# Kernel tuning notes

Hardware: AMD Instinct MI355X
Metric: run time of the kernel (lower is better)

The kernel has to match this reference:

```python
import jax, jax.numpy as jnp
import numpy as np
import itertools
jax.config.update("jax_enable_x64", True)

ND, NQ, B = 4, 3, 256          # ndrives, nqubits, batch_size
D = 2 ** NQ                     # Hilbert-space dim = 8


def _pauli_basis(nq):
    I = np.eye(2, dtype=np.complex128)
    X = np.array([[0, 1], [1, 0]], dtype=np.complex128)
    Y = np.array([[0, -1j], [1j, 0]], dtype=np.complex128)
    Z = np.array([[1, 0], [0, -1]], dtype=np.complex128)
    mats = []
    for combo in itertools.product([I, X, Y, Z], repeat=nq):
        m = np.array([[1.0 + 0j]], dtype=np.complex128)
        for s in combo:
            m = np.kron(m, s)
        mats.append(m)
    return np.stack(mats)  # [4**nq, 2**nq, 2**nq], Hermitian


def setup_inputs() -> dict:
    key = jax.random.key(0)
    k1, k2, k3 = jax.random.split(key, 3)
    paulies = jnp.asarray(_pauli_basis(NQ))          # [64, 8, 8] complex128
    L = paulies.shape[0]
    x = jax.random.normal(k1, (B, ND), dtype=jnp.float64)
    # keras 'normal' initializer ~ stddev 0.05
    kernel = 0.05 * jax.random.normal(k2, (ND, L), dtype=jnp.float64)
    bias = 0.05 * jax.random.normal(k3, (L,), dtype=jnp.float64)
    return {"x": x, "kernel": kernel, "bias": bias, "paulies": paulies}


def _probs(pw_i, paulies):
    # pw_i: [L] real pauli weights for one sample
    H = jnp.tensordot(pw_i.astype(jnp.complex128), paulies, axes=[[0], [0]])  # [D, D]
    e, v = jnp.linalg.eigh(H)                      # Hermitian eigendecomp
    expe = jnp.exp(-1j * e)                        # [D]
    # amp_j = sum_s conj(v)[0,s] * exp(-i e_s) * v[j,s]  (evolution of |0>)
    amp = jnp.einsum('s,js->j', jnp.conj(v[0, :]) * expe, v)  # [D]
    return amp.real ** 2 + amp.imag ** 2           # P, [D] float64


def reference(x, kernel, bias, paulies):
    pw = x @ kernel + bias                         # [B, L]
    f = lambda p: _probs(p, paulies)
    P = jax.vmap(f)(pw)                            # [B, D]
    # per-sample Jacobian dP/d(pauli_weights): [B, D, L]
    g = jax.vmap(jax.jacrev(f))(pw)
    oneoverp = 1.0 / P                             # [B, D]
    # chain rule: pw = x @ kernel + bias  =>  dP/dkernel[i,p,j,k] = x[i,j] * g[i,p,k]
    p_k = jnp.einsum('ij,ipk->ipjk', x, g)         # [B, D, ND, L]
    I_k = jnp.einsum('ipjk,iplm,ip->ijklm', p_k, p_k, oneoverp)  # [B, ND, L, ND, L]
    I_b = jnp.einsum('ipj,ipk,ip->ijk', g, g, oneoverp)          # [B, L, L]
    return (I_k, I_b)
```

## Files before the change

kernel.cpp:

```cpp
#include <hip/hip_runtime.h>
#include <math.h>

typedef float f4_t __attribute__((ext_vector_type(4)));

#define NTERM 26
#define TROW  9
#define TMAT  (TROW * 8)

__device__ __forceinline__ double rdin(const void* p, int idx, bool isdbl) {
  return isdbl ? ((const double*)p)[idx] : (double)((const float*)p)[idx];
}

__device__ __forceinline__ bool detect_dbl(const void* xv) {
  const float* xq = (const float*)xv;
  bool isdbl = false;
  for (int j = 0; j < 64; ++j) {
    float a = fabsf(xq[j]);
    if (!(a < 1e6f)) isdbl = true;
  }
  return isdbl;
}

__global__ __launch_bounds__(256) void fi_all(
    const void* __restrict__ xv,
    const void* __restrict__ kv,
    const void* __restrict__ bv,
    float* __restrict__ out, int Bn)
{
  const int wg   = blockIdx.x;
  const int i    = wg >> 2;
  const int jblk = wg & 3;
  const int t    = threadIdx.x;

  __shared__ float  pw[64];
  __shared__ float2 Zl[8][8];
  __shared__ float  invfact[56];
  __shared__ float2 Tall[NTERM * TMAT];
  __shared__ float2 Rl[NTERM][8];
  __shared__ float2 Ql[8][8][8];
  __shared__ float  ampre[8], ampim[8], invPs[8];
  __shared__ float  gk_t[8][64];
  __shared__ float  hk_t[8][68];

  const bool isdbl = detect_dbl(xv);

  if (t < 64) {
    float acc = (float)rdin(bv, t, isdbl);
    #pragma unroll
    for (int j = 0; j < 4; ++j)
      acc += (float)rdin(xv, i*4 + j, isdbl) * (float)rdin(kv, j*64 + t, isdbl);
    pw[t] = acc;
  } else if (t < 64 + 52) {
    int n = t - 64;
    float f = 1.0f;
    for (int u = 2; u <= n; ++u) f /= (float)u;
    invfact[n] = f;
  }
  __syncthreads();

  if (t < 64) {
    int r = t >> 3, c = t & 7;
    int m = r ^ c;
    float hre = 0.0f, him = 0.0f;
    for (int u = 0; u < 8; ++u) {
      int k = 0;
      float pr = 1.0f, pim = 0.0f;
      #pragma unroll
      for (int q = 0; q < 3; ++q) {
        int bit = 2 - q;
        int f  = (m >> bit) & 1;
        int ch = (u >> bit) & 1;
        int rb = (r >> bit) & 1;
        int d  = f ? (ch ? 2 : 1) : (ch ? 3 : 0);
        k = (k << 2) | d;
        if (d == 2) {
          float nr = rb ? -pim : pim;
          float ni = rb ?  pr  : -pr;
          pr = nr; pim = ni;
        } else if (d == 3 && rb) { pr = -pr; pim = -pim; }
      }
      float w = pw[k];
      hre += w * pr; him += w * pim;
    }
    Zl[r][c] = make_float2(him, -hre);
  }
  __syncthreads();

  if (t < 64) {
    const int r = t >> 3, c = t & 7;
    float2 Zrow[8];
    #pragma unroll
    for (int u = 0; u < 8; ++u) Zrow[u] = Zl[r][u];
    float Tre = (r == c) ? 1.0f : 0.0f;
    float Tim = 0.0f;
    Tall[r*TROW + c] = make_float2(Tre, Tim);
    #pragma unroll
    for (int j = 1; j < NTERM; ++j) {
      float cr[8], ci[8];
      #pragma unroll
      for (int u = 0; u < 8; ++u) {
        int srcl = (((u << 3) | c) << 2);
        cr[u] = __int_as_float(__builtin_amdgcn_ds_bpermute(srcl, __float_as_int(Tre)));
        ci[u] = __int_as_float(__builtin_amdgcn_ds_bpermute(srcl, __float_as_int(Tim)));
      }
      float nr = 0.0f, ni = 0.0f;
      #pragma unroll
      for (int u = 0; u < 8; ++u) {
        nr += Zrow[u].x*cr[u] - Zrow[u].y*ci[u];
        ni += Zrow[u].x*ci[u] + Zrow[u].y*cr[u];
      }
      Tre = nr; Tim = ni;
      Tall[j*TMAT + r*TROW + c] = make_float2(nr, ni);
    }
  }
  __syncthreads();

  if (t < NTERM * 8) {
    const int l = t >> 3, b = t & 7;
    float sr = 0.0f, si = 0.0f;
    for (int j = 0; j < NTERM; ++j) {
      float cf = invfact[j + l + 1];
      float2 a = Tall[j*TMAT + b*TROW];
      sr += cf * a.x; si += cf * a.y;
    }
    Rl[l][b] = make_float2(sr, si);
  }
  if (t < 8) {
    float ar = 0.0f, ai = 0.0f;
    for (int j = 0; j < NTERM; ++j) {
      float cf = invfact[j];
      float2 a = Tall[j*TMAT + t*TROW];
      ar += cf * a.x; ai += cf * a.y;
    }
    ampre[t] = ar; ampim[t] = ai;
    float P = ar*ar + ai*ai;
    invPs[t] = 1.0f / fmaxf(P, 1e-30f);
  }
  __syncthreads();

  {
    const int p  = t >> 5;
    const int a  = (t >> 2) & 7;
    const int b0 = (t & 3) << 1;
    float q0r = 0.f, q0i = 0.f, q1r = 0.f, q1i = 0.f;
    for (int l = 0; l < NTERM; ++l) {
      float2 T  = Tall[l*TMAT + p*TROW + a];
      float2 r0 = Rl[l][b0];
      float2 r1 = Rl[l][b0+1];
      q0r += T.x*r0.x - T.y*r0.y;  q0i += T.x*r0.y + T.y*r0.x;
      q1r += T.x*r1.x - T.y*r1.y;  q1i += T.x*r1.y + T.y*r1.x;
    }
    Ql[p][a][b0]   = make_float2(q0r, q0i);
    Ql[p][a][b0+1] = make_float2(q1r, q1i);
  }
  __syncthreads();

  if (t < 64) {
    const int k = t;
    const int d0 = (k >> 4) & 3, d1 = (k >> 2) & 3, d2 = k & 3;
    const int m = ((((d0 == 1) | (d0 == 2)) ? 1 : 0) << 2)
                | ((((d1 == 1) | (d1 == 2)) ? 1 : 0) << 1)
                |  (((d2 == 1) | (d2 == 2)) ? 1 : 0);
    float Sr[8], Si[8];
    #pragma unroll
    for (int p = 0; p < 8; ++p) { Sr[p] = 0.0f; Si[p] = 0.0f; }
    #pragma unroll
    for (int a = 0; a < 8; ++a) {
      float pr = 1.0f, pim = 0.0f;
      const int dd[3] = {d0, d1, d2};
      #pragma unroll
      for (int q = 0; q < 3; ++q) {
        int rb = (a >> (2 - q)) & 1;
        int d = dd[q];
        if (d == 2) {
          float nr = rb ? -pim : pim;
          float ni = rb ?  pr  : -pr;
          pr = nr; pim = ni;
        } else if (d == 3 && rb) { pr = -pr; pim = -pim; }
      }
      const int b = a ^ m;
      #pragma unroll
      for (int p = 0; p < 8; ++p) {
        float2 q2 = Ql[p][a][b];
        Sr[p] += pr*q2.x - pim*q2.y;
        Si[p] += pr*q2.y + pim*q2.x;
      }
    }
    #pragma unroll
    for (int p = 0; p < 8; ++p) {
      float gg = 2.0f * (ampre[p]*Si[p] - ampim[p]*Sr[p]);
      gk_t[p][k] = gg;
      hk_t[p][k] = gg * invPs[p];
    }
  }

  float xsc[4];
  {
    float xj = (float)rdin(xv, i*4 + jblk, isdbl);
    #pragma unroll
    for (int l = 0; l < 4; ++l)
      xsc[l] = xj * (float)rdin(xv, i*4 + l, isdbl);
  }
  __syncthreads();

  {
    const int m4  = (t & 15) << 2;
    const int g16 = t >> 4;
    float* okj = out + (size_t)i * 65536 + (size_t)jblk * 16384;
    float* ob  = out + (size_t)Bn * 65536 + (size_t)i * 4096;
    #pragma unroll
    for (int it = 0; it < 4; ++it) {
      const int k = it*16 + g16;
      f4_t acc = {0.f, 0.f, 0.f, 0.f};
      #pragma unroll
      for (int p = 0; p < 8; ++p) {
        float gv = gk_t[p][k];
        const f4_t hv = *(const f4_t*)&hk_t[p][m4];
        acc.x += gv*hv.x; acc.y += gv*hv.y; acc.z += gv*hv.z; acc.w += gv*hv.w;
      }
      if (jblk == 0)
        __builtin_nontemporal_store(acc, (f4_t*)(ob + (size_t)k*64 + m4));
      #pragma unroll
      for (int l = 0; l < 4; ++l) {
        f4_t vv = {xsc[l]*acc.x, xsc[l]*acc.y, xsc[l]*acc.z, xsc[l]*acc.w};
        __builtin_nontemporal_store(vv,
            (f4_t*)(okj + (size_t)k*256 + (size_t)l*64 + m4));
      }
    }
  }
}

extern "C" void kernel_launch(void* const* d_in, const int* in_sizes, int n_in,
                              void* d_out, int out_size, void* d_ws, size_t ws_size,
                              hipStream_t stream) {
  (void)n_in; (void)d_ws; (void)ws_size; (void)out_size;
  int Bn = in_sizes[0] / 4;
  fi_all<<<Bn * 4, 256, 0, stream>>>(d_in[0], d_in[1], d_in[2], (float*)d_out, Bn);
}
```

Baseline: 100.7 us.

## Cut Taylor terms, rotate solver wave per block, spread gradient stage over all waves

Reduces the Taylor series for the matrix exponential from 26 to 22 terms, which shrinks the serial T-power chain and the table sizes. Rotates which wavefront runs the serial setup so the four blocks per sample do not all load the same SIMD. Splits the gradient-contraction stage across all four waves, two Pauli rows each, instead of one wave doing all eight. The factorial loop now uses the hardware reciprocal. Fewer terms and the approximate reciprocal could cost accuracy if the Hamiltonian norm is large.

```diff
diff --git a/kernel.cpp b/kernel.cpp
--- a/kernel.cpp
+++ b/kernel.cpp
@@ -3,7 +3,7 @@
 
 typedef float f4_t __attribute__((ext_vector_type(4)));
 
-#define NTERM 26
+#define NTERM 22
 #define TROW  9
 #define TMAT  (TROW * 8)
 
@@ -31,10 +31,13 @@
   const int i    = wg >> 2;
   const int jblk = wg & 3;
   const int t    = threadIdx.x;
+  const int wv   = t >> 6;
+  const int tl   = t & 63;
+  const bool solver = (wv == jblk);
 
   __shared__ float  pw[64];
   __shared__ float2 Zl[8][8];
-  __shared__ float  invfact[56];
+  __shared__ float  invfact[48];
   __shared__ float2 Tall[NTERM * TMAT];
   __shared__ float2 Rl[NTERM][8];
   __shared__ float2 Ql[8][8][8];
@@ -44,22 +47,22 @@
 
   const bool isdbl = detect_dbl(xv);
 
-  if (t < 64) {
-    float acc = (float)rdin(bv, t, isdbl);
+  if (solver) {
+    float acc = (float)rdin(bv, tl, isdbl);
     #pragma unroll
     for (int j = 0; j < 4; ++j)
-      acc += (float)rdin(xv, i*4 + j, isdbl) * (float)rdin(kv, j*64 + t, isdbl);
-    pw[t] = acc;
-  } else if (t < 64 + 52) {
-    int n = t - 64;
+      acc += (float)rdin(xv, i*4 + j, isdbl) * (float)rdin(kv, j*64 + tl, isdbl);
+    pw[tl] = acc;
+  } else if (wv == ((jblk + 1) & 3) && tl < 48) {
+    int n = tl;
     float f = 1.0f;
-    for (int u = 2; u <= n; ++u) f /= (float)u;
+    for (int u = 2; u <= n; ++u) f *= __builtin_amdgcn_rcpf((float)u);
     invfact[n] = f;
   }
   __syncthreads();
 
-  if (t < 64) {
-    int r = t >> 3, c = t & 7;
+  if (solver) {
+    int r = tl >> 3, c = tl & 7;
     int m = r ^ c;
     float hre = 0.0f, him = 0.0f;
     for (int u = 0; u < 8; ++u) {
@@ -86,8 +89,8 @@
   }
   __syncthreads();
 
-  if (t < 64) {
-    const int r = t >> 3, c = t & 7;
+  if (solver) {
+    const int r = tl >> 3, c = tl & 7;
     float2 Zrow[8];
     #pragma unroll
     for (int u = 0; u < 8; ++u) Zrow[u] = Zl[r][u];
@@ -125,16 +128,17 @@
     }
     Rl[l][b] = make_float2(sr, si);
   }
-  if (t < 8) {
+  if (t >= 192 && t < 200) {
+    const int b = t - 192;
     float ar = 0.0f, ai = 0.0f;
     for (int j = 0; j < NTERM; ++j) {
       float cf = invfact[j];
-      float2 a = Tall[j*TMAT + t*TROW];
+      float2 a = Tall[j*TMAT + b*TROW];
       ar += cf * a.x; ai += cf * a.y;
     }
-    ampre[t] = ar; ampim[t] = ai;
+    ampre[b] = ar; ampim[b] = ai;
     float P = ar*ar + ai*ai;
-    invPs[t] = 1.0f / fmaxf(P, 1e-30f);
+    invPs[b] = 1.0f / fmaxf(P, 1e-30f);
   }
   __syncthreads();
 
@@ -155,15 +159,15 @@
   }
   __syncthreads();
 
-  if (t < 64) {
-    const int k = t;
+  {
+    const int k  = t & 63;
+    const int pg = t >> 6;
+    const int p0 = pg << 1, p1 = p0 + 1;
     const int d0 = (k >> 4) & 3, d1 = (k >> 2) & 3, d2 = k & 3;
     const int m = ((((d0 == 1) | (d0 == 2)) ? 1 : 0) << 2)
                 | ((((d1 == 1) | (d1 == 2)) ? 1 : 0) << 1)
                 |  (((d2 == 1) | (d2 == 2)) ? 1 : 0);
-    float Sr[8], Si[8];
-    #pragma unroll
-    for (int p = 0; p < 8; ++p) { Sr[p] = 0.0f; Si[p] = 0.0f; }
+    float S0r = 0.f, S0i = 0.f, S1r = 0.f, S1i = 0.f;
     #pragma unroll
     for (int a = 0; a < 8; ++a) {
       float pr = 1.0f, pim = 0.0f;
@@ -179,19 +183,15 @@
         } else if (d == 3 && rb) { pr = -pr; pim = -pim; }
       }
       const int b = a ^ m;
-      #pragma unroll
-      for (int p = 0; p < 8; ++p) {
-        float2 q2 = Ql[p][a][b];
-        Sr[p] += pr*q2.x - pim*q2.y;
-        Si[p] += pr*q2.y + pim*q2.x;
-      }
-    }
-    #pragma unroll
-    for (int p = 0; p < 8; ++p) {
-      float gg = 2.0f * (ampre[p]*Si[p] - ampim[p]*Sr[p]);
-      gk_t[p][k] = gg;
-      hk_t[p][k] = gg * invPs[p];
-    }
+      float2 qa = Ql[p0][a][b];
+      float2 qb = Ql[p1][a][b];
+      S0r += pr*qa.x - pim*qa.y;  S0i += pr*qa.y + pim*qa.x;
+      S1r += pr*qb.x - pim*qb.y;  S1i += pr*qb.y + pim*qb.x;
+    }
+    float g0 = 2.0f * (ampre[p0]*S0i - ampim[p0]*S0r);
+    float g1 = 2.0f * (ampre[p1]*S1i - ampim[p1]*S1r);
+    gk_t[p0][k] = g0;  hk_t[p0][k] = g0 * invPs[p0];
+    gk_t[p1][k] = g1;  hk_t[p1][k] = g1 * invPs[p1];
   }
 
   float xsc[4];
```

New measurement: 98.06 us. -2.6%, faster.
